# Performance work log

Measured on AMD Instinct MI355X. Metric: run time of the kernel, lower is better.

## Reference

```python
import jax, jax.numpy as jnp
import numpy as np

B, T, N, D, E = 16, 12, 512, 128, 32  # batch, time, nodes, model_dim, node_emb_dim


def setup_inputs() -> dict:
    key = jax.random.key(0)
    ks = jax.random.split(key, 7)
    return {
        "value": jax.random.normal(ks[0], (B, T, N, D), dtype=jnp.float32),
        "emb": jax.random.normal(ks[1], (T, N, E), dtype=jnp.float32),
        "attn_mask": jax.random.randint(ks[2], (B, N, N), 0, 2, dtype=jnp.int32),
        "W_qk": jax.random.normal(ks[3], (E, D), dtype=jnp.float32) * (1.0 / np.sqrt(E)),
        "b_qk": jax.random.normal(ks[4], (D,), dtype=jnp.float32) * 0.02,
        "W_v": jax.random.normal(ks[5], (D, D), dtype=jnp.float32) * (1.0 / np.sqrt(D)),
        "b_v": jax.random.normal(ks[6], (D,), dtype=jnp.float32) * 0.02,
    }


def reference(value, emb, attn_mask, W_qk, b_qk, W_v, b_v):
    # qk projection shared between query and key: [T, N, D]
    qk = emb @ W_qk + b_qk
    # query: softmax over feature dim D
    q = jax.nn.softmax(qk, axis=-1)                      # [T, N, D]
    # key: transpose then softmax over node dim N
    k = jax.nn.softmax(jnp.swapaxes(qk, -1, -2), axis=-1)  # [T, D, N]
    # value projection (note: out_proj in __init__ is unused in forward)
    v = value @ W_v + b_v                                # [B, T, N, D]
    # batch-independent base attention score, then broadcast over batch
    score = jnp.einsum('tnd,tdm->tnm', q, k)             # [T, N, N]
    score = jnp.broadcast_to(score[None], (value.shape[0],) + score.shape)  # [B, T, N, N]
    # masked fill: mask [B, N, N] -> [B, 1, N, N]
    score = jnp.where(attn_mask[:, None] == 0, jnp.float32(-1e9), score)
    out = jnp.einsum('btnm,btmd->btnd', score, v)         # [B, T, N, D]
    return out
```

## Files before the change

### kernel.cpp

```cpp
#include <hip/hip_runtime.h>

#define B_ 16
#define T_ 12
#define N_ 512
#define D_ 128
#define E_ 32

typedef __attribute__((ext_vector_type(8))) unsigned short u16x8;
typedef __attribute__((ext_vector_type(8))) __bf16 bf16x8;
typedef __attribute__((ext_vector_type(4))) float f32x4;

static __device__ __forceinline__ unsigned short f2bf(float f) {
    unsigned u = __float_as_uint(f);
    unsigned r = (u + 0x7fffu + ((u >> 16) & 1u)) >> 16;
    return (unsigned short)r;
}

static __device__ __forceinline__ void gld16(const void* src, void* dst) {
    __builtin_amdgcn_global_load_lds(
        (const __attribute__((address_space(1))) unsigned*)src,
        (__attribute__((address_space(3))) unsigned*)dst, 16, 0, 0);
}

__global__ __launch_bounds__(128) void kA1(const float* __restrict__ emb,
                                           const float* __restrict__ Wqk,
                                           const float* __restrict__ bqk,
                                           float* __restrict__ qk,
                                           unsigned short* __restrict__ qb,
                                           const float* __restrict__ Wv,
                                           unsigned short* __restrict__ WvT,
                                           const int* __restrict__ mask,
                                           unsigned* __restrict__ mb) {
    int bid = blockIdx.x;
    int tid = threadIdx.x;
    if (bid >= 896) {
        int o = (bid - 896) * 128 + tid;
        const int* mp = mask + (size_t)o * 32;
        unsigned bits = 0;
#pragma unroll
        for (int j = 0; j < 32; j += 4) {
            int4 m4 = *(const int4*)&mp[j];
            bits |= (m4.x ? 1u : 0u) << j;
            bits |= (m4.y ? 1u : 0u) << (j + 1);
            bits |= (m4.z ? 1u : 0u) << (j + 2);
            bits |= (m4.w ? 1u : 0u) << (j + 3);
        }
        mb[o] = bits;
        return;
    }
    if (bid >= 768) {
        int i = (bid - 768) * 128 + tid;
        int d = i >> 7, k = i & 127;
        WvT[d * 128 + k] = f2bf(Wv[k * 128 + d]);
        return;
    }
    int w = tid >> 6, l = tid & 63;
    float wq0[E_], wq1[E_];
#pragma unroll
    for (int e = 0; e < E_; ++e) {
        wq0[e] = Wqk[e * D_ + l];
        wq1[e] = Wqk[e * D_ + l + 64];
    }
    float b0 = bqk[l], b1 = bqk[l + 64];
    for (int rr = 0; rr < 4; ++rr) {
        int tn = bid * 8 + w * 4 + rr;
        const float* ep = emb + (size_t)tn * E_;
        float a0 = b0, a1 = b1;
#pragma unroll
        for (int e = 0; e < E_; ++e) {
            float ev = ep[e];
            a0 = fmaf(ev, wq0[e], a0);
            a1 = fmaf(ev, wq1[e], a1);
        }
        qk[(size_t)tn * D_ + l] = a0;
        qk[(size_t)tn * D_ + l + 64] = a1;
        float mx = fmaxf(a0, a1);
#pragma unroll
        for (int s = 32; s > 0; s >>= 1) mx = fmaxf(mx, __shfl_xor(mx, s));
        float e0 = __expf(a0 - mx), e1 = __expf(a1 - mx);
        float sum = e0 + e1;
#pragma unroll
        for (int s = 32; s > 0; s >>= 1) sum += __shfl_xor(sum, s);
        float inv = 1.f / sum;
        qb[(size_t)tn * D_ + l] = f2bf(e0 * inv);
        qb[(size_t)tn * D_ + l + 64] = f2bf(e1 * inv);
    }
}

__global__ __launch_bounds__(256) void kA2n(const float* __restrict__ qk,
                                            unsigned short* __restrict__ kN) {
    int t = blockIdx.x >> 4;
    int d0 = (blockIdx.x & 15) * 8;
    int tid = threadIdx.x;
    int dc = tid & 7, ni = tid >> 3;
    const float* base = qk + (size_t)t * N_ * D_ + d0 + dc;
    float vals[16];
    float mx = -1e30f;
#pragma unroll
    for (int j = 0; j < 16; ++j) {
        vals[j] = base[(size_t)(ni + 32 * j) * D_];
        mx = fmaxf(mx, vals[j]);
    }
#pragma unroll
    for (int s = 8; s < 64; s <<= 1) mx = fmaxf(mx, __shfl_xor(mx, s));
    __shared__ float red[2][4][8];
    int wv = tid >> 6;
    if ((tid & 63) < 8) red[0][wv][dc] = mx;
    __syncthreads();
    mx = fmaxf(fmaxf(red[0][0][dc], red[0][1][dc]),
               fmaxf(red[0][2][dc], red[0][3][dc]));
    float sum = 0.f;
#pragma unroll
    for (int j = 0; j < 16; ++j) {
        vals[j] = __expf(vals[j] - mx);
        sum += vals[j];
    }
#pragma unroll
    for (int s = 8; s < 64; s <<= 1) sum += __shfl_xor(sum, s);
    if ((tid & 63) < 8) red[1][wv][dc] = sum;
    __syncthreads();
    sum = red[1][0][dc] + red[1][1][dc] + red[1][2][dc] + red[1][3][dc];
    float inv = 1.f / sum;
    unsigned short* op = kN + (size_t)t * N_ * D_ + d0 + dc;
#pragma unroll
    for (int j = 0; j < 16; ++j)
        op[(size_t)(ni + 32 * j) * D_] = f2bf(vals[j] * inv);
}

__global__ __launch_bounds__(256, 2) void kF(const unsigned short* __restrict__ qb,
                                             const unsigned short* __restrict__ kN,
                                             unsigned short* __restrict__ sc,
                                             const float* __restrict__ value,
                                             const unsigned short* __restrict__ WvT,
                                             const float* __restrict__ bv,
                                             unsigned short* __restrict__ vT) {
    __shared__ unsigned short shA[128 * 128];
    __shared__ unsigned short shB[128 * 128];
    int bid = blockIdx.x;
    int tid = threadIdx.x;
    int wave = tid >> 6, lane = tid & 63;
    int q = lane >> 4, lr = lane & 15;
    int rbase = (wave & 1) * 64, cbase = (wave >> 1) * 64;
    int il = lane >> 4, i16 = lane & 15;

    f32x4 acc[4][4];
#pragma unroll
    for (int i = 0; i < 4; ++i)
#pragma unroll
        for (int j = 0; j < 4; ++j) acc[i][j] = (f32x4){0.f, 0.f, 0.f, 0.f};

    if (bid < 192) {
        int mt = bid & 3, nt = (bid >> 2) & 3, t = bid >> 4;
        int n0 = nt * 128, m0 = mt * 128;
        const char* qp = (const char*)(qb + (size_t)t * N_ * D_ + (size_t)n0 * D_);
        const char* kp = (const char*)(kN + (size_t)t * N_ * D_ + (size_t)m0 * D_);
#pragma unroll
        for (int it = 0; it < 8; ++it) {
            int r = it * 16 + wave * 4 + il;
            int si = (i16 * 16) ^ ((r & 15) << 4);
            char* dA = (char*)shA + (it * 16 + wave * 4) * 256 + lane * 16;
            char* dB = (char*)shB + (it * 16 + wave * 4) * 256 + lane * 16;
            gld16(qp + (size_t)r * 256 + si, dA);
            gld16(kp + (size_t)r * 256 + si, dB);
        }
        asm volatile("s_waitcnt vmcnt(0)" ::: "memory");
        __builtin_amdgcn_s_barrier();
        const char* Ab = (const char*)shA;
        const char* Bb = (const char*)shB;
#pragma unroll
        for (int ks = 0; ks < 4; ++ks) {
            bf16x8 a[4], b[4];
#pragma unroll
            for (int i = 0; i < 4; ++i) {
                int r = rbase + 16 * i + lr;
                a[i] = *(const bf16x8*)(Ab + r * 256 + ((ks * 64 + q * 16) ^ ((r & 15) << 4)));
            }
#pragma unroll
            for (int j = 0; j < 4; ++j) {
                int r = cbase + 16 * j + lr;
                b[j] = *(const bf16x8*)(Bb + r * 256 + ((ks * 64 + q * 16) ^ ((r & 15) << 4)));
            }
#pragma unroll
            for (int i = 0; i < 4; ++i)
#pragma unroll
                for (int j = 0; j < 4; ++j)
                    acc[i][j] = __builtin_amdgcn_mfma_f32_16x16x32_bf16(
                        a[i], b[j], acc[i][j], 0, 0, 0);
        }
        unsigned short* sp = sc + (size_t)t * N_ * N_;
#pragma unroll
        for (int i = 0; i < 4; ++i)
#pragma unroll
            for (int j = 0; j < 4; ++j) {
                int row0 = n0 + rbase + 16 * i + q * 4;
                int col = m0 + cbase + 16 * j + lr;
#pragma unroll
                for (int e = 0; e < 4; ++e)
                    sp[(size_t)(row0 + e) * N_ + col] = f2bf(acc[i][j][e]);
            }
        return;
    }

    {
        int idx = bid - 192;
        int mt = idx & 3, bt = idx >> 2;
        int m0 = mt * 128;
        const float* vp = value + ((size_t)bt * N_ + m0) * D_;
        const char* wp = (const char*)WvT;

        int g = tid >> 4, c16 = tid & 15;
        float4 vv[16];
#pragma unroll
        for (int j = 0; j < 16; ++j) {
            int r = g * 8 + (j >> 1);
            int kf = (j & 1) * 64 + c16 * 4;
            vv[j] = *(const float4*)(vp + (size_t)r * D_ + kf);
        }
#pragma unroll
        for (int it = 0; it < 8; ++it) {
            int r = it * 16 + wave * 4 + il;
            int si = (i16 * 16) ^ ((r & 15) << 4);
            char* dA = (char*)shA + (it * 16 + wave * 4) * 256 + lane * 16;
            gld16(wp + (size_t)r * 256 + si, dA);
        }
#pragma unroll
        for (int j = 0; j < 16; ++j) {
            int r = g * 8 + (j >> 1);
            int kb = (j & 1) * 128 + c16 * 8;
            ushort4 o;
            o.x = f2bf(vv[j].x); o.y = f2bf(vv[j].y);
            o.z = f2bf(vv[j].z); o.w = f2bf(vv[j].w);
            *(ushort4*)((char*)shB + r * 256 + (kb ^ ((r & 15) << 4))) = o;
        }
        asm volatile("s_waitcnt vmcnt(0) lgkmcnt(0)" ::: "memory");
        __builtin_amdgcn_s_barrier();
        const char* Ab = (const char*)shA;
        const char* Bb = (const char*)shB;
#pragma unroll
        for (int ks = 0; ks < 4; ++ks) {
            bf16x8 a[4], b[4];
#pragma unroll
            for (int i = 0; i < 4; ++i) {
                int r = rbase + 16 * i + lr;
                a[i] = *(const bf16x8*)(Ab + r * 256 + ((ks * 64 + q * 16) ^ ((r & 15) << 4)));
            }
#pragma unroll
            for (int j = 0; j < 4; ++j) {
                int r = cbase + 16 * j + lr;
                b[j] = *(const bf16x8*)(Bb + r * 256 + ((ks * 64 + q * 16) ^ ((r & 15) << 4)));
            }
#pragma unroll
            for (int i = 0; i < 4; ++i)
#pragma unroll
                for (int j = 0; j < 4; ++j)
                    acc[i][j] = __builtin_amdgcn_mfma_f32_16x16x32_bf16(
                        a[i], b[j], acc[i][j], 0, 0, 0);
        }
        unsigned short* op = vT + (size_t)bt * N_ * D_;
#pragma unroll
        for (int i = 0; i < 4; ++i) {
            int row0 = rbase + 16 * i + q * 4;
            float4 bq = *(const float4*)&bv[row0];
#pragma unroll
            for (int j = 0; j < 4; ++j) {
                int col = m0 + cbase + 16 * j + lr;
                op[(size_t)(row0 + 0) * N_ + col] = f2bf(acc[i][j][0] + bq.x);
                op[(size_t)(row0 + 1) * N_ + col] = f2bf(acc[i][j][1] + bq.y);
                op[(size_t)(row0 + 2) * N_ + col] = f2bf(acc[i][j][2] + bq.z);
                op[(size_t)(row0 + 3) * N_ + col] = f2bf(acc[i][j][3] + bq.w);
            }
        }
    }
}

__global__ __launch_bounds__(256, 3) void kC(const unsigned short* __restrict__ sc,
                                             const unsigned* __restrict__ mb,
                                             const unsigned short* __restrict__ vT,
                                             float* __restrict__ out) {
    int n0 = blockIdx.x * 128;
    int t = blockIdx.y, b = blockIdx.z;
    int tid = threadIdx.x;
    int wave = tid >> 6, lane = tid & 63;
    int q = lane >> 4, lr = lane & 15;
    int rbase = (wave & 1) * 64, cbase = (wave >> 1) * 64;

    __shared__ unsigned short Sb[128 * 64];
    __shared__ unsigned short Vb[2][128 * 64];

    const unsigned short* scp = sc + (size_t)t * N_ * N_ + (size_t)n0 * N_;
    const unsigned short* vtp = vT + ((size_t)(b * T_ + t)) * N_ * D_;
    const unsigned* mbp = mb + ((size_t)b * N_ + n0) * 16;
    const unsigned short NEG = 0xCE6E;

    f32x4 acc[4][4];
#pragma unroll
    for (int i = 0; i < 4; ++i)
#pragma unroll
        for (int j = 0; j < 4; ++j) acc[i][j] = (f32x4){0.f, 0.f, 0.f, 0.f};

    int sr = tid >> 1, sh2 = tid & 1;
    const unsigned short* sg = scp + (size_t)sr * N_ + sh2 * 32;
    const unsigned* mwp = mbp + sr * 16 + sh2;
    int swz_r = (sr & 7) << 4;
    char* Sw[4];
#pragma unroll
    for (int p = 0; p < 4; ++p)
        Sw[p] = (char*)Sb + sr * 128 + ((sh2 * 64 + p * 16) ^ swz_r);

    int l3 = lane >> 3, l7 = lane & 7;
    int vin = (l7 * 16) ^ (l3 << 4);
    const char* vbase = (const char*)vtp;

#pragma unroll
    for (int it = 0; it < 4; ++it) {
        int row = (it * 4 + wave) * 8 + l3;
        const char* src = vbase + (size_t)row * 1024 + vin;
        char* dst = (char*)&Vb[0][0] + ((it * 4 + wave) * 64 + lane) * 16;
        gld16(src, dst);
    }
    u16x8 sreg[4];
    unsigned mw;
#pragma unroll
    for (int p = 0; p < 4; ++p) sreg[p] = *(const u16x8*)(sg + p * 8);
    mw = mwp[0];

    for (int kc = 0; kc < 8; ++kc) {
        int cur = kc & 1;
#pragma unroll
        for (int p = 0; p < 4; ++p) {
            unsigned bits = mw >> (p * 8);
            u16x8 o;
#pragma unroll
            for (int j = 0; j < 8; ++j)
                o[j] = ((bits >> j) & 1u) ? sreg[p][j] : NEG;
            *(u16x8*)Sw[p] = o;
        }
        if (kc < 7) {
            int off = (kc + 1) * 128;
#pragma unroll
            for (int it = 0; it < 4; ++it) {
                int row = (it * 4 + wave) * 8 + l3;
                const char* src = vbase + (size_t)row * 1024 + off + vin;
                char* dst = (char*)&Vb[cur ^ 1][0] + ((it * 4 + wave) * 64 + lane) * 16;
                gld16(src, dst);
            }
            int eoff = (kc + 1) * 64;
#pragma unroll
            for (int p = 0; p < 4; ++p) sreg[p] = *(const u16x8*)(sg + eoff + p * 8);
            mw = mwp[(kc + 1) * 2];
        }
        asm volatile("s_waitcnt lgkmcnt(0)" ::: "memory");
        __builtin_amdgcn_s_barrier();
        __builtin_amdgcn_sched_barrier(0);
        {
            const char* Sbase = (const char*)Sb;
            const char* Vbase = (const char*)&Vb[cur][0];
            int swz_l = (lr & 7) << 4;
#pragma unroll
            for (int ks = 0; ks < 2; ++ks) {
                bf16x8 a[4], bb[4];
#pragma unroll
                for (int i = 0; i < 4; ++i) {
                    int r = rbase + 16 * i + lr;
                    a[i] = *(const bf16x8*)(Sbase + r * 128 + ((ks * 64 + q * 16) ^ swz_l));
                }
#pragma unroll
                for (int j = 0; j < 4; ++j) {
                    int d = cbase + 16 * j + lr;
                    bb[j] = *(const bf16x8*)(Vbase + d * 128 + ((ks * 64 + q * 16) ^ swz_l));
                }
#pragma unroll
                for (int i = 0; i < 4; ++i)
#pragma unroll
                    for (int j = 0; j < 4; ++j)
                        acc[i][j] = __builtin_amdgcn_mfma_f32_16x16x32_bf16(
                            a[i], bb[j], acc[i][j], 0, 0, 0);
            }
        }
        __builtin_amdgcn_s_barrier();
        __builtin_amdgcn_sched_barrier(0);
    }

    float* ob = out + ((size_t)(b * T_ + t)) * N_ * D_;
#pragma unroll
    for (int i = 0; i < 4; ++i) {
#pragma unroll
        for (int j = 0; j < 4; ++j) {
            int row0 = n0 + rbase + 16 * i + q * 4;
            int col = cbase + 16 * j + lr;
#pragma unroll
            for (int e = 0; e < 4; ++e)
                ob[(size_t)(row0 + e) * D_ + col] = acc[i][j][e];
        }
    }
}

extern "C" void kernel_launch(void* const* d_in, const int* in_sizes, int n_in,
                              void* d_out, int out_size, void* d_ws, size_t ws_size,
                              hipStream_t stream) {
    const float* value = (const float*)d_in[0];
    const float* emb   = (const float*)d_in[1];
    const int*   mask  = (const int*)d_in[2];
    const float* Wqk   = (const float*)d_in[3];
    const float* bqk   = (const float*)d_in[4];
    const float* Wv    = (const float*)d_in[5];
    const float* bvv   = (const float*)d_in[6];
    float* out = (float*)d_out;

    float* ws = (float*)d_ws;
    float*          qkf  = ws;
    unsigned short* qb   = (unsigned short*)(ws + 786432);
    unsigned short* kNb  = (unsigned short*)(ws + 1179648);
    unsigned short* scb  = (unsigned short*)(ws + 1572864);
    unsigned short* vtb  = (unsigned short*)(ws + 3145728);
    unsigned short* WvTb = (unsigned short*)(ws + 9437184);
    unsigned*       mbp  = (unsigned*)(ws + 9445376);

    kA1<<<1920, 128, 0, stream>>>(emb, Wqk, bqk, qkf, qb, Wv, WvTb, mask, mbp);
    kA2n<<<192, 256, 0, stream>>>(qkf, kNb);
    kF<<<960, 256, 0, stream>>>(qb, kNb, scb, value, WvTb, bvv, vtb);
    kC<<<dim3(4, T_, B_), 256, 0, stream>>>(scb, mbp, vtb, out);
}
```

Measured before the change: 160.5 us.

## Fuse key softmax into first kernel and split kF staging into two K chunks

Merges the qk projection and the column softmax for keys into one kernel. Each block recomputes its qk column slice from emb staged in LDS, so the fp32 qk buffer and the separate kA2n launch are no longer needed. The kF GEMM kernel now stages A/B in two K-halves with partial waitcnt, so MFMA on the first half overlaps the loads of the second. This adds redundant projection compute and more barriers in exchange for one fewer launch and less global traffic.

```diff
diff --git a/kernel.cpp b/kernel.cpp
--- a/kernel.cpp
+++ b/kernel.cpp
@@ -22,19 +22,146 @@
         (__attribute__((address_space(3))) unsigned*)dst, 16, 0, 0);
 }
 
-__global__ __launch_bounds__(128) void kA1(const float* __restrict__ emb,
-                                           const float* __restrict__ Wqk,
-                                           const float* __restrict__ bqk,
-                                           float* __restrict__ qk,
-                                           unsigned short* __restrict__ qb,
-                                           const float* __restrict__ Wv,
-                                           unsigned short* __restrict__ WvT,
-                                           const int* __restrict__ mask,
-                                           unsigned* __restrict__ mb) {
+__global__ __launch_bounds__(256) void k1(const float* __restrict__ emb,
+                                          const float* __restrict__ Wqk,
+                                          const float* __restrict__ bqk,
+                                          unsigned short* __restrict__ qb,
+                                          unsigned short* __restrict__ kN,
+                                          const float* __restrict__ Wv,
+                                          unsigned short* __restrict__ WvT,
+                                          const int* __restrict__ mask,
+                                          unsigned* __restrict__ mb) {
+    __shared__ __align__(16) char LE[256 * 128];
+    __shared__ float red[2][4][8];
     int bid = blockIdx.x;
     int tid = threadIdx.x;
-    if (bid >= 896) {
-        int o = (bid - 896) * 128 + tid;
+
+    if (bid < 192) {
+        int t = bid >> 4;
+        int d0 = (bid & 15) * 8;
+        int dc = tid & 7, ni = tid >> 3;
+        float wqv[E_];
+#pragma unroll
+        for (int e = 0; e < E_; ++e) wqv[e] = Wqk[e * D_ + d0 + dc];
+        float bq = bqk[d0 + dc];
+        const float4* eb4 = (const float4*)(emb + (size_t)t * N_ * E_);
+
+        float4 st0[8], st1[8];
+#pragma unroll
+        for (int ii = 0; ii < 8; ++ii) st0[ii] = eb4[ii * 256 + tid];
+#pragma unroll
+        for (int ii = 0; ii < 8; ++ii) {
+            int f = ii * 256 + tid;
+            int n = f >> 3, s = f & 7;
+            *(float4*)(LE + n * 128 + ((s * 16) ^ ((n & 7) << 4))) = st0[ii];
+        }
+#pragma unroll
+        for (int ii = 0; ii < 8; ++ii) st1[ii] = eb4[2048 + ii * 256 + tid];
+        __syncthreads();
+
+        float vals[16];
+#pragma unroll
+        for (int jj = 0; jj < 8; ++jj) {
+            int n = ni + 32 * jj;
+            float a = bq;
+#pragma unroll
+            for (int s = 0; s < 8; ++s) {
+                f32x4 ev = *(const f32x4*)(LE + n * 128 + ((s * 16) ^ ((n & 7) << 4)));
+                a = fmaf(ev[0], wqv[s * 4 + 0], a);
+                a = fmaf(ev[1], wqv[s * 4 + 1], a);
+                a = fmaf(ev[2], wqv[s * 4 + 2], a);
+                a = fmaf(ev[3], wqv[s * 4 + 3], a);
+            }
+            vals[jj] = a;
+        }
+        __syncthreads();
+#pragma unroll
+        for (int ii = 0; ii < 8; ++ii) {
+            int f = ii * 256 + tid;
+            int n = f >> 3, s = f & 7;
+            *(float4*)(LE + n * 128 + ((s * 16) ^ ((n & 7) << 4))) = st1[ii];
+        }
+        __syncthreads();
+#pragma unroll
+        for (int jj = 0; jj < 8; ++jj) {
+            int n = ni + 32 * jj;
+            float a = bq;
+#pragma unroll
+            for (int s = 0; s < 8; ++s) {
+                f32x4 ev = *(const f32x4*)(LE + n * 128 + ((s * 16) ^ ((n & 7) << 4)));
+                a = fmaf(ev[0], wqv[s * 4 + 0], a);
+                a = fmaf(ev[1], wqv[s * 4 + 1], a);
+                a = fmaf(ev[2], wqv[s * 4 + 2], a);
+                a = fmaf(ev[3], wqv[s * 4 + 3], a);
+            }
+            vals[8 + jj] = a;
+        }
+
+        float mx = -1e30f;
+#pragma unroll
+        for (int j = 0; j < 16; ++j) mx = fmaxf(mx, vals[j]);
+#pragma unroll
+        for (int s = 8; s < 64; s <<= 1) mx = fmaxf(mx, __shfl_xor(mx, s));
+        int wv = tid >> 6;
+        if ((tid & 63) < 8) red[0][wv][dc] = mx;
+        __syncthreads();
+        mx = fmaxf(fmaxf(red[0][0][dc], red[0][1][dc]),
+                   fmaxf(red[0][2][dc], red[0][3][dc]));
+        float sum = 0.f;
+#pragma unroll
+        for (int j = 0; j < 16; ++j) {
+            vals[j] = __expf(vals[j] - mx);
+            sum += vals[j];
+        }
+#pragma unroll
+        for (int s = 8; s < 64; s <<= 1) sum += __shfl_xor(sum, s);
+        if ((tid & 63) < 8) red[1][wv][dc] = sum;
+        __syncthreads();
+        sum = red[1][0][dc] + red[1][1][dc] + red[1][2][dc] + red[1][3][dc];
+        float inv = 1.f / sum;
+        unsigned short* op = kN + (size_t)t * N_ * D_ + d0 + dc;
+#pragma unroll
+        for (int j = 0; j < 16; ++j)
+            op[(size_t)(ni + 32 * j) * D_] = f2bf(vals[j] * inv);
+        return;
+    }
+
+    if (bid < 576) {
+        int bid2 = bid - 192;
+        int w = tid >> 6, l = tid & 63;
+        float wq0[E_], wq1[E_];
+#pragma unroll
+        for (int e = 0; e < E_; ++e) {
+            wq0[e] = Wqk[e * D_ + l];
+            wq1[e] = Wqk[e * D_ + l + 64];
+        }
+        float b0 = bqk[l], b1 = bqk[l + 64];
+        for (int rr = 0; rr < 4; ++rr) {
+            int tn = bid2 * 16 + w * 4 + rr;
+            const float* ep = emb + (size_t)tn * E_;
+            float a0 = b0, a1 = b1;
+#pragma unroll
+            for (int e = 0; e < E_; ++e) {
+                float ev = ep[e];
+                a0 = fmaf(ev, wq0[e], a0);
+                a1 = fmaf(ev, wq1[e], a1);
+            }
+            float mx = fmaxf(a0, a1);
+#pragma unroll
+            for (int s = 32; s > 0; s >>= 1) mx = fmaxf(mx, __shfl_xor(mx, s));
+            float e0 = __expf(a0 - mx), e1 = __expf(a1 - mx);
+            float sum = e0 + e1;
+#pragma unroll
+            for (int s = 32; s > 0; s >>= 1) sum += __shfl_xor(sum, s);
+            float inv = 1.f / sum;
+            qb[(size_t)tn * D_ + l] = f2bf(e0 * inv);
+            qb[(size_t)tn * D_ + l + 64] = f2bf(e1 * inv);
+        }
+        return;
+    }
+
+    if (bid < 1088) {
+        int o = (bid - 576) * 256 + tid;
         const int* mp = mask + (size_t)o * 32;
         unsigned bits = 0;
 #pragma unroll
@@ -48,83 +175,12 @@
         mb[o] = bits;
         return;
     }
-    if (bid >= 768) {
-        int i = (bid - 768) * 128 + tid;
+
+    {
+        int i = (bid - 1088) * 256 + tid;
         int d = i >> 7, k = i & 127;
         WvT[d * 128 + k] = f2bf(Wv[k * 128 + d]);
-        return;
-    }
-    int w = tid >> 6, l = tid & 63;
-    float wq0[E_], wq1[E_];
-#pragma unroll
-    for (int e = 0; e < E_; ++e) {
-        wq0[e] = Wqk[e * D_ + l];
-        wq1[e] = Wqk[e * D_ + l + 64];
-    }
-    float b0 = bqk[l], b1 = bqk[l + 64];
-    for (int rr = 0; rr < 4; ++rr) {
-        int tn = bid * 8 + w * 4 + rr;
-        const float* ep = emb + (size_t)tn * E_;
-        float a0 = b0, a1 = b1;
-#pragma unroll
-        for (int e = 0; e < E_; ++e) {
-            float ev = ep[e];
-            a0 = fmaf(ev, wq0[e], a0);
-            a1 = fmaf(ev, wq1[e], a1);
-        }
-        qk[(size_t)tn * D_ + l] = a0;
-        qk[(size_t)tn * D_ + l + 64] = a1;
-        float mx = fmaxf(a0, a1);
-#pragma unroll
-        for (int s = 32; s > 0; s >>= 1) mx = fmaxf(mx, __shfl_xor(mx, s));
-        float e0 = __expf(a0 - mx), e1 = __expf(a1 - mx);
-        float sum = e0 + e1;
-#pragma unroll
-        for (int s = 32; s > 0; s >>= 1) sum += __shfl_xor(sum, s);
-        float inv = 1.f / sum;
-        qb[(size_t)tn * D_ + l] = f2bf(e0 * inv);
-        qb[(size_t)tn * D_ + l + 64] = f2bf(e1 * inv);
-    }
-}
-
-__global__ __launch_bounds__(256) void kA2n(const float* __restrict__ qk,
-                                            unsigned short* __restrict__ kN) {
-    int t = blockIdx.x >> 4;
-    int d0 = (blockIdx.x & 15) * 8;
-    int tid = threadIdx.x;
-    int dc = tid & 7, ni = tid >> 3;
-    const float* base = qk + (size_t)t * N_ * D_ + d0 + dc;
-    float vals[16];
-    float mx = -1e30f;
-#pragma unroll
-    for (int j = 0; j < 16; ++j) {
-        vals[j] = base[(size_t)(ni + 32 * j) * D_];
-        mx = fmaxf(mx, vals[j]);
-    }
-#pragma unroll
-    for (int s = 8; s < 64; s <<= 1) mx = fmaxf(mx, __shfl_xor(mx, s));
-    __shared__ float red[2][4][8];
-    int wv = tid >> 6;
-    if ((tid & 63) < 8) red[0][wv][dc] = mx;
-    __syncthreads();
-    mx = fmaxf(fmaxf(red[0][0][dc], red[0][1][dc]),
-               fmaxf(red[0][2][dc], red[0][3][dc]));
-    float sum = 0.f;
-#pragma unroll
-    for (int j = 0; j < 16; ++j) {
-        vals[j] = __expf(vals[j] - mx);
-        sum += vals[j];
-    }
-#pragma unroll
-    for (int s = 8; s < 64; s <<= 1) sum += __shfl_xor(sum, s);
-    if ((tid & 63) < 8) red[1][wv][dc] = sum;
-    __syncthreads();
-    sum = red[1][0][dc] + red[1][1][dc] + red[1][2][dc] + red[1][3][dc];
-    float inv = 1.f / sum;
-    unsigned short* op = kN + (size_t)t * N_ * D_ + d0 + dc;
-#pragma unroll
-    for (int j = 0; j < 16; ++j)
-        op[(size_t)(ni + 32 * j) * D_] = f2bf(vals[j] * inv);
+    }
 }
 
 __global__ __launch_bounds__(256, 2) void kF(const unsigned short* __restrict__ qb,
@@ -134,59 +190,68 @@
                                              const unsigned short* __restrict__ WvT,
                                              const float* __restrict__ bv,
                                              unsigned short* __restrict__ vT) {
-    __shared__ unsigned short shA[128 * 128];
-    __shared__ unsigned short shB[128 * 128];
+    __shared__ __align__(16) char LA[2][128 * 128];
+    __shared__ __align__(16) char LB[2][128 * 128];
     int bid = blockIdx.x;
     int tid = threadIdx.x;
     int wave = tid >> 6, lane = tid & 63;
     int q = lane >> 4, lr = lane & 15;
     int rbase = (wave & 1) * 64, cbase = (wave >> 1) * 64;
-    int il = lane >> 4, i16 = lane & 15;
+    int l3 = lane >> 3, l7 = lane & 7;
 
     f32x4 acc[4][4];
 #pragma unroll
     for (int i = 0; i < 4; ++i)
 #pragma unroll
         for (int j = 0; j < 4; ++j) acc[i][j] = (f32x4){0.f, 0.f, 0.f, 0.f};
+
+#define STAGE_T(gbase, lb, c)                                                   \
+    _Pragma("unroll") for (int it_ = 0; it_ < 4; ++it_) {                       \
+        int row_ = it_ * 32 + wave * 8 + l3;                                    \
+        gld16((gbase) + (size_t)row_ * 256 + (c) * 128 +                        \
+                  ((l7 * 16) ^ ((row_ & 7) << 4)),                              \
+              (lb) + (it_ * 32 + wave * 8) * 128 + lane * 16);                  \
+    }
+
+#define MFMA_CHUNK(c)                                                           \
+    _Pragma("unroll") for (int ksl_ = 0; ksl_ < 2; ++ksl_) {                    \
+        bf16x8 a_[4], b_[4];                                                    \
+        _Pragma("unroll") for (int i_ = 0; i_ < 4; ++i_) {                      \
+            int r_ = rbase + 16 * i_ + lr;                                      \
+            a_[i_] = *(const bf16x8*)(LA[c] + r_ * 128 +                        \
+                                      ((ksl_ * 64 + q * 16) ^ ((r_ & 7) << 4)));\
+        }                                                                       \
+        _Pragma("unroll") for (int j_ = 0; j_ < 4; ++j_) {                      \
+            int r_ = cbase + 16 * j_ + lr;                                      \
+            b_[j_] = *(const bf16x8*)(LB[c] + r_ * 128 +                        \
+                                      ((ksl_ * 64 + q * 16) ^ ((r_ & 7) << 4)));\
+        }                                                                       \
+        _Pragma("unroll") for (int i_ = 0; i_ < 4; ++i_)                        \
+            _Pragma("unroll") for (int j_ = 0; j_ < 4; ++j_)                    \
+                acc[i_][j_] = __builtin_amdgcn_mfma_f32_16x16x32_bf16(          \
+                    a_[i_], b_[j_], acc[i_][j_], 0, 0, 0);                      \
+    }
 
     if (bid < 192) {
         int mt = bid & 3, nt = (bid >> 2) & 3, t = bid >> 4;
         int n0 = nt * 128, m0 = mt * 128;
         const char* qp = (const char*)(qb + (size_t)t * N_ * D_ + (size_t)n0 * D_);
         const char* kp = (const char*)(kN + (size_t)t * N_ * D_ + (size_t)m0 * D_);
-#pragma unroll
-        for (int it = 0; it < 8; ++it) {
-            int r = it * 16 + wave * 4 + il;
-            int si = (i16 * 16) ^ ((r & 15) << 4);
-            char* dA = (char*)shA + (it * 16 + wave * 4) * 256 + lane * 16;
-            char* dB = (char*)shB + (it * 16 + wave * 4) * 256 + lane * 16;
-            gld16(qp + (size_t)r * 256 + si, dA);
-            gld16(kp + (size_t)r * 256 + si, dB);
-        }
+        STAGE_T(qp, LA[0], 0)
+        STAGE_T(kp, LB[0], 0)
+        STAGE_T(qp, LA[1], 1)
+        STAGE_T(kp, LB[1], 1)
+        asm volatile("s_waitcnt vmcnt(8)" ::: "memory");
+        __builtin_amdgcn_sched_barrier(0);
+        __builtin_amdgcn_s_barrier();
+        __builtin_amdgcn_sched_barrier(0);
+        MFMA_CHUNK(0)
         asm volatile("s_waitcnt vmcnt(0)" ::: "memory");
-        __builtin_amdgcn_s_barrier();
-        const char* Ab = (const char*)shA;
-        const char* Bb = (const char*)shB;
-#pragma unroll
-        for (int ks = 0; ks < 4; ++ks) {
-            bf16x8 a[4], b[4];
-#pragma unroll
-            for (int i = 0; i < 4; ++i) {
-                int r = rbase + 16 * i + lr;
-                a[i] = *(const bf16x8*)(Ab + r * 256 + ((ks * 64 + q * 16) ^ ((r & 15) << 4)));
-            }
-#pragma unroll
-            for (int j = 0; j < 4; ++j) {
-                int r = cbase + 16 * j + lr;
-                b[j] = *(const bf16x8*)(Bb + r * 256 + ((ks * 64 + q * 16) ^ ((r & 15) << 4)));
-            }
-#pragma unroll
-            for (int i = 0; i < 4; ++i)
-#pragma unroll
-                for (int j = 0; j < 4; ++j)
-                    acc[i][j] = __builtin_amdgcn_mfma_f32_16x16x32_bf16(
-                        a[i], b[j], acc[i][j], 0, 0, 0);
-        }
+        __builtin_amdgcn_sched_barrier(0);
+        __builtin_amdgcn_s_barrier();
+        __builtin_amdgcn_sched_barrier(0);
+        MFMA_CHUNK(1)
+
         unsigned short* sp = sc + (size_t)t * N_ * N_;
 #pragma unroll
         for (int i = 0; i < 4; ++i)
@@ -207,55 +272,49 @@
         int m0 = mt * 128;
         const float* vp = value + ((size_t)bt * N_ + m0) * D_;
         const char* wp = (const char*)WvT;
-
         int g = tid >> 4, c16 = tid & 15;
-        float4 vv[16];
-#pragma unroll
-        for (int j = 0; j < 16; ++j) {
-            int r = g * 8 + (j >> 1);
-            int kf = (j & 1) * 64 + c16 * 4;
-            vv[j] = *(const float4*)(vp + (size_t)r * D_ + kf);
-        }
-#pragma unroll
-        for (int it = 0; it < 8; ++it) {
-            int r = it * 16 + wave * 4 + il;
-            int si = (i16 * 16) ^ ((r & 15) << 4);
-            char* dA = (char*)shA + (it * 16 + wave * 4) * 256 + lane * 16;
-            gld16(wp + (size_t)r * 256 + si, dA);
-        }
-#pragma unroll
-        for (int j = 0; j < 16; ++j) {
-            int r = g * 8 + (j >> 1);
-            int kb = (j & 1) * 128 + c16 * 8;
+
+        float4 v0[8], v1[8];
+#pragma unroll
+        for (int jj = 0; jj < 8; ++jj)
+            v0[jj] = *(const float4*)(vp + (size_t)(g * 8 + jj) * D_ + c16 * 4);
+        __builtin_amdgcn_sched_barrier(0);
+        STAGE_T(wp, LA[0], 0)
+        __builtin_amdgcn_sched_barrier(0);
+#pragma unroll
+        for (int jj = 0; jj < 8; ++jj)
+            v1[jj] = *(const float4*)(vp + (size_t)(g * 8 + jj) * D_ + 64 + c16 * 4);
+        __builtin_amdgcn_sched_barrier(0);
+        STAGE_T(wp, LA[1], 1)
+        __builtin_amdgcn_sched_barrier(0);
+
+#pragma unroll
+        for (int jj = 0; jj < 8; ++jj) {
+            int row = g * 8 + jj;
             ushort4 o;
-            o.x = f2bf(vv[j].x); o.y = f2bf(vv[j].y);
-            o.z = f2bf(vv[j].z); o.w = f2bf(vv[j].w);
-            *(ushort4*)((char*)shB + r * 256 + (kb ^ ((r & 15) << 4))) = o;
+            o.x = f2bf(v0[jj].x); o.y = f2bf(v0[jj].y);
+            o.z = f2bf(v0[jj].z); o.w = f2bf(v0[jj].w);
+            *(ushort4*)(LB[0] + row * 128 + ((c16 * 8) ^ ((row & 7) << 4))) = o;
+        }
+        asm volatile("s_waitcnt vmcnt(12) lgkmcnt(0)" ::: "memory");
+        __builtin_amdgcn_sched_barrier(0);
+        __builtin_amdgcn_s_barrier();
+        __builtin_amdgcn_sched_barrier(0);
+        MFMA_CHUNK(0)
+#pragma unroll
+        for (int jj = 0; jj < 8; ++jj) {
+            int row = g * 8 + jj;
+            ushort4 o;
+            o.x = f2bf(v1[jj].x); o.y = f2bf(v1[jj].y);
+            o.z = f2bf(v1[jj].z); o.w = f2bf(v1[jj].w);
+            *(ushort4*)(LB[1] + row * 128 + ((c16 * 8) ^ ((row & 7) << 4))) = o;
         }
         asm volatile("s_waitcnt vmcnt(0) lgkmcnt(0)" ::: "memory");
-        __builtin_amdgcn_s_barrier();
-        const char* Ab = (const char*)shA;
-        const char* Bb = (const char*)shB;
-#pragma unroll
-        for (int ks = 0; ks < 4; ++ks) {
-            bf16x8 a[4], b[4];
-#pragma unroll
-            for (int i = 0; i < 4; ++i) {
-                int r = rbase + 16 * i + lr;
-                a[i] = *(const bf16x8*)(Ab + r * 256 + ((ks * 64 + q * 16) ^ ((r & 15) << 4)));
-            }
-#pragma unroll
-            for (int j = 0; j < 4; ++j) {
-                int r = cbase + 16 * j + lr;
-                b[j] = *(const bf16x8*)(Bb + r * 256 + ((ks * 64 + q * 16) ^ ((r & 15) << 4)));
-            }
-#pragma unroll
-            for (int i = 0; i < 4; ++i)
-#pragma unroll
-                for (int j = 0; j < 4; ++j)
-                    acc[i][j] = __builtin_amdgcn_mfma_f32_16x16x32_bf16(
-                        a[i], b[j], acc[i][j], 0, 0, 0);
-        }
+        __builtin_amdgcn_sched_barrier(0);
+        __builtin_amdgcn_s_barrier();
+        __builtin_amdgcn_sched_barrier(0);
+        MFMA_CHUNK(1)
+
         unsigned short* op = vT + (size_t)bt * N_ * D_;
 #pragma unroll
         for (int i = 0; i < 4; ++i) {
@@ -271,6 +330,8 @@
             }
         }
     }
+#undef STAGE_T
+#undef MFMA_CHUNK
 }
 
 __global__ __launch_bounds__(256, 3) void kC(const unsigned short* __restrict__ sc,
@@ -408,7 +469,6 @@
     float* out = (float*)d_out;
 
     float* ws = (float*)d_ws;
-    float*          qkf  = ws;
     unsigned short* qb   = (unsigned short*)(ws + 786432);
     unsigned short* kNb  = (unsigned short*)(ws + 1179648);
     unsigned short* scb  = (unsigned short*)(ws + 1572864);
@@ -416,8 +476,7 @@
     unsigned short* WvTb = (unsigned short*)(ws + 9437184);
     unsigned*       mbp  = (unsigned*)(ws + 9445376);
 
-    kA1<<<1920, 128, 0, stream>>>(emb, Wqk, bqk, qkf, qb, Wv, WvTb, mask, mbp);
-    kA2n<<<192, 256, 0, stream>>>(qkf, kNb);
+    k1<<<1152, 256, 0, stream>>>(emb, Wqk, bqk, qb, kNb, Wv, WvTb, mask, mbp);
     kF<<<960, 256, 0, stream>>>(qb, kNb, scb, value, WvTb, bvv, vtb);
     kC<<<dim3(4, T_, B_), 256, 0, stream>>>(scb, mbp, vtb, out);
 }
```

Result: faster. 157.3 us (-2.0%).
